# Kernel optimization log

Hardware: AMD Instinct MI355X
Metric: run time of the kernel (lower is better)

The kernel has to match this reference:

```python
import jax, jax.numpy as jnp
import numpy as np

DIM = 1024
N_HEADS = 16
HEAD_DIM = DIM // N_HEADS
LN_EPS = 1e-5


def layer_norm(x, gamma, beta, eps=LN_EPS):
    mu = jnp.mean(x, axis=-1, keepdims=True)
    var = jnp.var(x, axis=-1, keepdims=True)
    return (x - mu) * jax.lax.rsqrt(var + eps) * gamma + beta


def setup_inputs() -> dict:
    key = jax.random.key(0)
    ks = jax.random.split(key, 12)
    B, Nq, Nc, D = 2, 1024, 4096, DIM
    s = 1.0 / np.sqrt(D)  # torch Linear default init scale (uniform bound)
    inp = {
        "query": jax.random.normal(ks[0], (B, Nq, D), jnp.float32),
        "context": jax.random.normal(ks[1], (B, Nc, D), jnp.float32),
        "wq": jax.random.uniform(ks[2], (D, D), jnp.float32, -s, s),
        "bq": jax.random.uniform(ks[3], (D,), jnp.float32, -s, s),
        "wk": jax.random.uniform(ks[4], (D, D), jnp.float32, -s, s),
        "bk": jax.random.uniform(ks[5], (D,), jnp.float32, -s, s),
        "wv": jax.random.uniform(ks[6], (D, D), jnp.float32, -s, s),
        "bv": jax.random.uniform(ks[7], (D,), jnp.float32, -s, s),
        "wo": jax.random.uniform(ks[8], (D, D), jnp.float32, -s, s),
        "bo": jax.random.uniform(ks[9], (D,), jnp.float32, -s, s),
        "g_q": jnp.ones((D,), jnp.float32),
        "b_q": jnp.zeros((D,), jnp.float32),
        "g_kv": jnp.ones((D,), jnp.float32),
        "b_kv": jnp.zeros((D,), jnp.float32),
    }
    return inp


def reference(query, context, wq, bq, wk, bk, wv, bv, wo, bo, g_q, b_q, g_kv, b_kv):
    B, Nq, D = query.shape
    Nc = context.shape[1]
    H, Hd = N_HEADS, HEAD_DIM

    qn = layer_norm(query, g_q, b_q)        # [B,Nq,D]
    cn = layer_norm(context, g_kv, b_kv)    # [B,Nc,D]

    # torch Linear: y = x @ W.T + b; weights here stored as [out,in]
    Q = (jnp.einsum('bnd,ed->bne', qn, wq) + bq).reshape(B, Nq, H, Hd)
    K = (jnp.einsum('bnd,ed->bne', cn, wk) + bk).reshape(B, Nc, H, Hd)
    V = (jnp.einsum('bnd,ed->bne', cn, wv) + bv).reshape(B, Nc, H, Hd)

    scale = 1.0 / np.sqrt(Hd)
    scores = jnp.einsum('bqhd,bkhd->bhqk', Q, K) * scale  # [B,H,Nq,Nc]
    attn = jax.nn.softmax(scores, axis=-1)
    out = jnp.einsum('bhqk,bkhd->bqhd', attn, V).reshape(B, Nq, D)

    return qn + (jnp.einsum('bnd,ed->bne', out, wo) + bo)
```

## Files before the change

### kernel.cpp

```cpp
#include <hip/hip_runtime.h>

typedef unsigned short u16;
typedef __attribute__((ext_vector_type(8))) __bf16 bf16x8;
typedef __attribute__((ext_vector_type(4))) float f32x4;

struct alignas(8) U16x4 { u16 x, y, z, w; };

#define MFMA16(a, b, c) __builtin_amdgcn_mfma_f32_16x16x32_bf16(a, b, c, 0, 0, 0)

__device__ __forceinline__ u16 f2bf(float f) {
    union { float f; unsigned u; } v; v.f = f;
    unsigned r = v.u + 0x7fffu + ((v.u >> 16) & 1u);
    return (u16)(r >> 16);
}

__device__ __forceinline__ unsigned cvt_pk_bf16(float lo, float hi) {
    unsigned r;
    asm("v_cvt_pk_bf16_f32 %0, %1, %2" : "=v"(r) : "v"(lo), "v"(hi));
    return r;
}

__device__ __forceinline__ float fexp2(float x) {
    float r;
    asm("v_exp_f32 %0, %1" : "=v"(r) : "v"(x));
    return r;
}

__device__ __forceinline__ void gload_lds16(const void* g, void* l) {
    __builtin_amdgcn_global_load_lds(
        (__attribute__((address_space(1))) void*)g,
        (__attribute__((address_space(3))) void*)l, 16, 0, 0);
}

__global__ __launch_bounds__(256)
void prep(const float* __restrict__ query, const float* __restrict__ context,
          const float* __restrict__ g_q, const float* __restrict__ b_q,
          const float* __restrict__ g_kv, const float* __restrict__ b_kv,
          float* __restrict__ qn32, u16* __restrict__ qnb, u16* __restrict__ cnb,
          const float4* __restrict__ w0, const float4* __restrict__ w1,
          const float4* __restrict__ w2, const float4* __restrict__ w3,
          U16x4* __restrict__ o0, U16x4* __restrict__ o1,
          U16x4* __restrict__ o2, U16x4* __restrict__ o3)
{
    const int blk = blockIdx.x;
    if (blk < 2560) {
        const float *x, *g, *be; float* y32; u16* y16; int rb;
        if (blk < 512) { x = query;   g = g_q;  be = b_q;  y32 = qn32;    y16 = qnb; rb = blk; }
        else           { x = context; g = g_kv; be = b_kv; y32 = nullptr; y16 = cnb; rb = blk - 512; }
        const int wid = threadIdx.x >> 6, lane = threadIdx.x & 63;
        const size_t row = (size_t)rb * 4 + wid;
        const float4* xr = (const float4*)(x + row * 1024);
        float4 v[4];
        float s = 0.f, ss = 0.f;
#pragma unroll
        for (int i = 0; i < 4; ++i) {
            v[i] = xr[i * 64 + lane];
            s  += (v[i].x + v[i].y) + (v[i].z + v[i].w);
            ss += (v[i].x * v[i].x + v[i].y * v[i].y) + (v[i].z * v[i].z + v[i].w * v[i].w);
        }
#pragma unroll
        for (int o = 32; o; o >>= 1) { s += __shfl_xor(s, o, 64); ss += __shfl_xor(ss, o, 64); }
        const float mu = s * (1.f / 1024.f);
        const float rstd = rsqrtf(ss * (1.f / 1024.f) - mu * mu + 1e-5f);
#pragma unroll
        for (int i = 0; i < 4; ++i) {
            float4 gv = ((const float4*)g)[i * 64 + lane];
            float4 bv = ((const float4*)be)[i * 64 + lane];
            float4 o;
            o.x = (v[i].x - mu) * rstd * gv.x + bv.x;
            o.y = (v[i].y - mu) * rstd * gv.y + bv.y;
            o.z = (v[i].z - mu) * rstd * gv.z + bv.z;
            o.w = (v[i].w - mu) * rstd * gv.w + bv.w;
            if (y32) ((float4*)(y32 + row * 1024))[i * 64 + lane] = o;
            U16x4 pk = { f2bf(o.x), f2bf(o.y), f2bf(o.z), f2bf(o.w) };
            ((U16x4*)(y16 + row * 1024))[i * 64 + lane] = pk;
        }
    } else {
        const int i = (blk - 2560) * 256 + threadIdx.x;
        float4 v;
        v = w0[i]; o0[i] = { f2bf(v.x), f2bf(v.y), f2bf(v.z), f2bf(v.w) };
        v = w1[i]; o1[i] = { f2bf(v.x), f2bf(v.y), f2bf(v.z), f2bf(v.w) };
        v = w2[i]; o2[i] = { f2bf(v.x), f2bf(v.y), f2bf(v.z), f2bf(v.w) };
        v = w3[i]; o3[i] = { f2bf(v.x), f2bf(v.y), f2bf(v.z), f2bf(v.w) };
    }
}

__global__ __launch_bounds__(512, 4)
void gemm_kv(const u16* __restrict__ A, const u16* __restrict__ Wk,
             const u16* __restrict__ Wv, const float* __restrict__ bkp,
             const float* __restrict__ bvp, u16* __restrict__ Kout,
             u16* __restrict__ Vt)
{
    constexpr int K = 1024, N = 1024, BK = 64;
    __shared__ __align__(16) u16 sA[128 * BK];
    __shared__ __align__(16) u16 sK[128 * BK];
    __shared__ __align__(16) u16 sV[128 * BK];
    const int tid = threadIdx.x, wid = tid >> 6, lane = tid & 63;
    const int lr = lane & 15, lg = lane >> 4;
    const int wr = wid >> 2, wc = wid & 3;
    const int row0 = blockIdx.x * 128, col0 = blockIdx.y * 128;
    const int srow = wid * 8 + (lane >> 3), scol = (lane & 7) * 8;

    const u16* Ag = A  + (size_t)(row0 + srow) * K + scol;
    const u16* Kg = Wk + (size_t)(col0 + srow) * K + scol;
    const u16* Vg = Wv + (size_t)(col0 + srow) * K + scol;

    f32x4 ka[4][2], va[4][2];
#pragma unroll
    for (int m = 0; m < 4; ++m)
#pragma unroll
        for (int n = 0; n < 2; ++n) {
            ka[m][n] = (f32x4){0.f, 0.f, 0.f, 0.f};
            va[m][n] = (f32x4){0.f, 0.f, 0.f, 0.f};
        }

    for (int k0 = 0; k0 < K; k0 += BK) {
        __syncthreads();
#pragma unroll
        for (int i = 0; i < 2; ++i) {
            gload_lds16(Ag + (size_t)i * 64 * K + k0, (char*)sA + i * 8192 + wid * 1024);
            gload_lds16(Kg + (size_t)i * 64 * K + k0, (char*)sK + i * 8192 + wid * 1024);
            gload_lds16(Vg + (size_t)i * 64 * K + k0, (char*)sV + i * 8192 + wid * 1024);
        }
        __syncthreads();
#pragma unroll
        for (int kk = 0; kk < 2; ++kk) {
            bf16x8 af[4], bk[2], bv[2];
#pragma unroll
            for (int m = 0; m < 4; ++m)
                af[m] = *(const bf16x8*)&sA[(wr * 64 + m * 16 + lr) * BK + kk * 32 + lg * 8];
#pragma unroll
            for (int n = 0; n < 2; ++n) {
                bk[n] = *(const bf16x8*)&sK[(wc * 32 + n * 16 + lr) * BK + kk * 32 + lg * 8];
                bv[n] = *(const bf16x8*)&sV[(wc * 32 + n * 16 + lr) * BK + kk * 32 + lg * 8];
            }
#pragma unroll
            for (int m = 0; m < 4; ++m)
#pragma unroll
                for (int n = 0; n < 2; ++n) {
                    ka[m][n] = MFMA16(af[m], bk[n], ka[m][n]);
                    va[m][n] = MFMA16(af[m], bv[n], va[m][n]);
                }
        }
    }

#pragma unroll
    for (int m = 0; m < 4; ++m) {
#pragma unroll
        for (int n = 0; n < 2; ++n) {
            const int r = row0 + wr * 64 + m * 16 + lg * 4;
            const int c = col0 + wc * 32 + n * 16 + lr;
            const float kb = bkp[c], vb = bvp[c];
#pragma unroll
            for (int j = 0; j < 4; ++j)
                Kout[(size_t)(r + j) * N + c] = f2bf(ka[m][n][j] + kb);
            const size_t base = ((size_t)(r >> 12) * 1024 + c) * 4096 + (r & 4095);
            U16x4 pk = { f2bf(va[m][n][0] + vb), f2bf(va[m][n][1] + vb),
                         f2bf(va[m][n][2] + vb), f2bf(va[m][n][3] + vb) };
            *(U16x4*)&Vt[base] = pk;
        }
    }
}

template<int MODE>
__global__ __launch_bounds__(256)
void gemm_bt64(const u16* __restrict__ A, const u16* __restrict__ W,
               const float* __restrict__ bias, const float* __restrict__ resid,
               void* __restrict__ Cp, int M, int N, int K, float alpha)
{
    constexpr int BK = 64;
    __shared__ __align__(16) u16 sA[64 * BK];
    __shared__ __align__(16) u16 sB[128 * BK];
    const int tid = threadIdx.x, wid = tid >> 6, lane = tid & 63;
    const int lr = lane & 15, lg = lane >> 4;
    const int wr = wid >> 1, wc = wid & 1;
    const int row0 = blockIdx.x * 64, col0 = blockIdx.y * 128;
    const int srow = wid * 8 + (lane >> 3), scol = (lane & 7) * 8;

    const u16* Ag = A + (size_t)(row0 + srow) * K + scol;
    const u16* Wg = W + (size_t)(col0 + srow) * K + scol;

    f32x4 acc[2][4];
#pragma unroll
    for (int m = 0; m < 2; ++m)
#pragma unroll
        for (int n = 0; n < 4; ++n) acc[m][n] = (f32x4){0.f, 0.f, 0.f, 0.f};

    for (int k0 = 0; k0 < K; k0 += BK) {
        __syncthreads();
#pragma unroll
        for (int i = 0; i < 2; ++i)
            gload_lds16(Ag + (size_t)i * 32 * K + k0, (char*)sA + i * 4096 + wid * 1024);
#pragma unroll
        for (int i = 0; i < 4; ++i)
            gload_lds16(Wg + (size_t)i * 32 * K + k0, (char*)sB + i * 4096 + wid * 1024);
        __syncthreads();
#pragma unroll
        for (int kk = 0; kk < 2; ++kk) {
            bf16x8 af[2], bfr[4];
#pragma unroll
            for (int m = 0; m < 2; ++m)
                af[m] = *(const bf16x8*)&sA[(wr * 32 + m * 16 + lr) * BK + kk * 32 + lg * 8];
#pragma unroll
            for (int n = 0; n < 4; ++n)
                bfr[n] = *(const bf16x8*)&sB[(wc * 64 + n * 16 + lr) * BK + kk * 32 + lg * 8];
#pragma unroll
            for (int m = 0; m < 2; ++m)
#pragma unroll
                for (int n = 0; n < 4; ++n)
                    acc[m][n] = MFMA16(af[m], bfr[n], acc[m][n]);
        }
    }

#pragma unroll
    for (int m = 0; m < 2; ++m) {
#pragma unroll
        for (int n = 0; n < 4; ++n) {
            const int r = row0 + wr * 32 + m * 16 + lg * 4;
            const int c = col0 + wc * 64 + n * 16 + lr;
            const float bv = bias[c];
            if constexpr (MODE == 0) {
                u16* C = (u16*)Cp;
#pragma unroll
                for (int j = 0; j < 4; ++j)
                    C[(size_t)(r + j) * N + c] = f2bf((acc[m][n][j] + bv) * alpha);
            } else {
                float* C = (float*)Cp;
#pragma unroll
                for (int j = 0; j < 4; ++j)
                    C[(size_t)(r + j) * N + c] =
                        (acc[m][n][j] + bv) * alpha + resid[(size_t)(r + j) * N + c];
            }
        }
    }
}

__global__ __launch_bounds__(512, 4)
void attn_fwd(const u16* __restrict__ Q, const u16* __restrict__ Kg,
              const u16* __restrict__ Vt, u16* __restrict__ O)
{
    constexpr int D = 1024, CSTR = 19;
    __shared__ __align__(16) char smem[81920];

    const int tid = threadIdx.x, wid = tid >> 6, lane = tid & 63;
    const int grp = wid >> 2, w = wid & 3;
    const int lr = lane & 15, lg = lane >> 4;
    const int rs = lr & 7;
    const int pkey = (lr & 7) << 4;

    const int fid = blockIdx.x;
    const int wkid = (fid & 7) * 64 + (fid >> 3);
    const int qblk = wkid & 15, h = (wkid >> 4) & 15, b = wkid >> 8;
    const int q0 = qblk * 64 + w * 16;

    const u16* Qrow = Q + (size_t)(b * 1024 + q0 + lr) * D + h * 64;
    const bf16x8 qf0 = *(const bf16x8*)(Qrow + lg * 8);
    const bf16x8 qf1 = *(const bf16x8*)(Qrow + 32 + lg * 8);

    const int srow = w * 8 + (lane >> 3);
    const int scol = ((lane & 7) ^ (srow & 7)) * 8;
    const u16* kp = Kg + (size_t)(b * 4096 + grp * 2048 + srow) * D + h * 64 + scol;
    const u16* vp = Vt + ((size_t)(b * 16 + h) * 64 + srow) * 4096 + grp * 2048 + scol;

    char* sProw = smem + 65536 + wid * 2048 + lr * 128;

    f32x4 po[4];
#pragma unroll
    for (int df = 0; df < 4; ++df) po[df] = (f32x4){0.f, 0.f, 0.f, 0.f};
    float m = -INFINITY, l = 0.f;
    bf16x8 vr0, vr1, vr2, vr3, vr4, vr5, vr6, vr7;

    auto pv_step = [&]() {
        bf16x8 pf0 = *(const bf16x8*)(sProw + ((lg * 16) ^ pkey));
        bf16x8 pf1 = *(const bf16x8*)(sProw + ((64 + lg * 16) ^ pkey));
        po[0] = MFMA16(vr0, pf0, po[0]);
        po[1] = MFMA16(vr1, pf0, po[1]);
        po[2] = MFMA16(vr2, pf0, po[2]);
        po[3] = MFMA16(vr3, pf0, po[3]);
        po[0] = MFMA16(vr4, pf1, po[0]);
        po[1] = MFMA16(vr5, pf1, po[1]);
        po[2] = MFMA16(vr6, pf1, po[2]);
        po[3] = MFMA16(vr7, pf1, po[3]);
    };

    {
        char* kd = smem + grp * 8192 + w * 1024;
        char* vd = smem + 32768 + grp * 8192 + w * 1024;
        gload_lds16(kp,                      kd);
        gload_lds16(kp + (size_t)32 * D,     kd + 4096);
        gload_lds16(vp,                      vd);
        gload_lds16(vp + (size_t)32 * 4096,  vd + 4096);
        kp += (size_t)64 * D; vp += 64;
    }
    asm volatile("s_waitcnt vmcnt(0)" ::: "memory");
    asm volatile("s_barrier" ::: "memory");

    for (int t = 0; t < 32; ++t) {
        const int cur = t & 1;
        if (t < 31) {
            char* kd = smem + (cur ^ 1) * 16384 + grp * 8192 + w * 1024;
            char* vd = smem + 32768 + (cur ^ 1) * 16384 + grp * 8192 + w * 1024;
            gload_lds16(kp,                      kd);
            gload_lds16(kp + (size_t)32 * D,     kd + 4096);
            gload_lds16(vp,                      vd);
            gload_lds16(vp + (size_t)32 * 4096,  vd + 4096);
            kp += (size_t)64 * D; vp += 64;
        }

        const u16* kb = (const u16*)(smem + cur * 16384 + grp * 8192);
        const u16* vb = (const u16*)(smem + 32768 + cur * 16384 + grp * 8192);

        __builtin_amdgcn_s_setprio(1);
        if (t > 0) pv_step();

        f32x4 s4[4];
#pragma unroll
        for (int f = 0; f < 4; ++f) {
            const int r = f * 16 + lr;
            bf16x8 k0v = *(const bf16x8*)&kb[r * 64 + (lg ^ rs) * 8];
            bf16x8 k1v = *(const bf16x8*)&kb[r * 64 + ((lg + 4) ^ rs) * 8];
            f32x4 z = (f32x4){0.f, 0.f, 0.f, 0.f};
            z = MFMA16(k0v, qf0, z);
            s4[f] = MFMA16(k1v, qf1, z);
        }
        __builtin_amdgcn_s_setprio(0);

        vr0 = *(const bf16x8*)&vb[(0 * 16 + lr) * 64 + ((0 + lg) ^ rs) * 8];
        vr1 = *(const bf16x8*)&vb[(1 * 16 + lr) * 64 + ((0 + lg) ^ rs) * 8];
        vr2 = *(const bf16x8*)&vb[(2 * 16 + lr) * 64 + ((0 + lg) ^ rs) * 8];
        vr3 = *(const bf16x8*)&vb[(3 * 16 + lr) * 64 + ((0 + lg) ^ rs) * 8];
        vr4 = *(const bf16x8*)&vb[(0 * 16 + lr) * 64 + ((4 + lg) ^ rs) * 8];
        vr5 = *(const bf16x8*)&vb[(1 * 16 + lr) * 64 + ((4 + lg) ^ rs) * 8];
        vr6 = *(const bf16x8*)&vb[(2 * 16 + lr) * 64 + ((4 + lg) ^ rs) * 8];
        vr7 = *(const bf16x8*)&vb[(3 * 16 + lr) * 64 + ((4 + lg) ^ rs) * 8];

        float pmax = fmaxf(fmaxf(fmaxf(s4[0][0], s4[0][1]), fmaxf(s4[0][2], s4[0][3])),
                     fmaxf(fmaxf(fmaxf(s4[1][0], s4[1][1]), fmaxf(s4[1][2], s4[1][3])),
                     fmaxf(fmaxf(fmaxf(s4[2][0], s4[2][1]), fmaxf(s4[2][2], s4[2][3])),
                           fmaxf(fmaxf(s4[3][0], s4[3][1]), fmaxf(s4[3][2], s4[3][3])))));
        if (!__all(pmax <= m)) {
            float tmax = fmaxf(pmax, __shfl_xor(pmax, 16, 64));
            tmax = fmaxf(tmax, __shfl_xor(tmax, 32, 64));
            const float mn = fmaxf(m, tmax);
            const float corr = fexp2(m - mn);
            l *= corr;
#pragma unroll
            for (int df = 0; df < 4; ++df) po[df] *= corr;
            m = mn;
        }
        float lsum = 0.f;
        uint2 pk[4];
#pragma unroll
        for (int f = 0; f < 4; ++f) {
            float p0 = fexp2(s4[f][0] - m);
            float p1 = fexp2(s4[f][1] - m);
            float p2 = fexp2(s4[f][2] - m);
            float p3 = fexp2(s4[f][3] - m);
            lsum += (p0 + p1) + (p2 + p3);
            pk[f].x = cvt_pk_bf16(p0, p1);
            pk[f].y = cvt_pk_bf16(p2, p3);
        }
        l += lsum;

#pragma unroll
        for (int f = 0; f < 4; ++f)
            *(uint2*)(sProw + ((f * 32 + lg * 8) ^ pkey)) = pk[f];

        asm volatile("s_waitcnt vmcnt(0) lgkmcnt(0)" ::: "memory");
        asm volatile("s_barrier" ::: "memory");
    }

    pv_step();

    l += __shfl_xor(l, 16, 64);
    l += __shfl_xor(l, 32, 64);

    float* cb = (float*)smem;
    if (grp == 1) {
        float* dst = cb + (size_t)(w * 64 + lane) * CSTR;
        dst[0] = m; dst[1] = l;
#pragma unroll
        for (int df = 0; df < 4; ++df)
#pragma unroll
            for (int j = 0; j < 4; ++j) dst[2 + df * 4 + j] = po[df][j];
    }
    __syncthreads();
    if (grp == 0) {
        const float* src = cb + (size_t)(w * 64 + lane) * CSTR;
        const float m1 = src[0], l1 = src[1];
        const float M = fmaxf(m, m1);
        const float c0 = fexp2(m - M), c1 = fexp2(m1 - M);
        const float rl = 1.f / (l * c0 + l1 * c1);
        u16* Orow = O + (size_t)(b * 1024 + q0 + lr) * D + h * 64;
#pragma unroll
        for (int df = 0; df < 4; ++df) {
            U16x4 opk = { f2bf((po[df][0] * c0 + src[2 + df * 4 + 0] * c1) * rl),
                          f2bf((po[df][1] * c0 + src[2 + df * 4 + 1] * c1) * rl),
                          f2bf((po[df][2] * c0 + src[2 + df * 4 + 2] * c1) * rl),
                          f2bf((po[df][3] * c0 + src[2 + df * 4 + 3] * c1) * rl) };
            *(U16x4*)&Orow[df * 16 + lg * 4] = opk;
        }
    }
}

extern "C" void kernel_launch(void* const* d_in, const int* in_sizes, int n_in,
                              void* d_out, int out_size, void* d_ws, size_t ws_size,
                              hipStream_t stream)
{
    const float* query   = (const float*)d_in[0];
    const float* context = (const float*)d_in[1];
    const float* wq = (const float*)d_in[2];
    const float* bq = (const float*)d_in[3];
    const float* wk = (const float*)d_in[4];
    const float* bk = (const float*)d_in[5];
    const float* wv = (const float*)d_in[6];
    const float* bv = (const float*)d_in[7];
    const float* wo = (const float*)d_in[8];
    const float* bo = (const float*)d_in[9];
    const float* g_q  = (const float*)d_in[10];
    const float* b_q  = (const float*)d_in[11];
    const float* g_kv = (const float*)d_in[12];
    const float* b_kv = (const float*)d_in[13];

    char* p = (char*)d_ws;
    auto alloc = [&](size_t bytes) { char* r = p; p += (bytes + 255) & ~(size_t)255; return r; };
    u16*   wqb  = (u16*)alloc(1024 * 1024 * 2);
    u16*   wkb  = (u16*)alloc(1024 * 1024 * 2);
    u16*   wvb  = (u16*)alloc(1024 * 1024 * 2);
    u16*   wob  = (u16*)alloc(1024 * 1024 * 2);
    float* qn32 = (float*)alloc((size_t)2048 * 1024 * 4);
    u16*   qnb  = (u16*)alloc((size_t)2048 * 1024 * 2);
    u16*   cnb  = (u16*)alloc((size_t)8192 * 1024 * 2);
    u16*   Qb   = (u16*)alloc((size_t)2048 * 1024 * 2);
    u16*   Kb   = (u16*)alloc((size_t)8192 * 1024 * 2);
    u16*   Vtb  = (u16*)alloc((size_t)8192 * 1024 * 2);
    u16*   AOb  = (u16*)alloc((size_t)2048 * 1024 * 2);

    prep<<<3584, 256, 0, stream>>>(query, context, g_q, b_q, g_kv, b_kv,
                                   qn32, qnb, cnb,
                                   (const float4*)wq, (const float4*)wk,
                                   (const float4*)wv, (const float4*)wo,
                                   (U16x4*)wqb, (U16x4*)wkb, (U16x4*)wvb, (U16x4*)wob);

    gemm_bt64<0><<<dim3(32, 8), 256, 0, stream>>>(qnb, wqb, bq, nullptr, Qb, 2048, 1024, 1024, 0.18033688f);
    gemm_kv<<<dim3(64, 8), 512, 0, stream>>>(cnb, wkb, wvb, bk, bv, Kb, Vtb);

    attn_fwd<<<dim3(512), 512, 0, stream>>>(Qb, Kb, Vtb, AOb);

    gemm_bt64<1><<<dim3(32, 8), 256, 0, stream>>>(AOb, wob, bo, qn32, d_out, 2048, 1024, 1024, 1.0f);
}
```

Baseline: 164.6 us.

## Process two query tiles per wave in attention, halving block threads

Each wave in the attention kernel now handles 32 query rows (two 16-row tiles) instead of 16, with 4 waves per block instead of 8. Every K and V fragment read from shared memory is reused for two MFMAs, which cuts LDS traffic per FLOP. The software-pipelined PV step from the previous iteration is replaced by an in-iteration PV computation, so the s_setprio interleaving is dropped. In exchange, register pressure roughly doubles for the accumulators and there are fewer waves per CU to hide latency.

```diff
diff --git a/kernel.cpp b/kernel.cpp
--- a/kernel.cpp
+++ b/kernel.cpp
@@ -235,15 +235,15 @@
     }
 }
 
-__global__ __launch_bounds__(512, 4)
+__global__ __launch_bounds__(256, 2)
 void attn_fwd(const u16* __restrict__ Q, const u16* __restrict__ Kg,
               const u16* __restrict__ Vt, u16* __restrict__ O)
 {
-    constexpr int D = 1024, CSTR = 19;
+    constexpr int D = 1024, CSTR = 36;
     __shared__ __align__(16) char smem[81920];
 
     const int tid = threadIdx.x, wid = tid >> 6, lane = tid & 63;
-    const int grp = wid >> 2, w = wid & 3;
+    const int grp = wid >> 1, w = wid & 1;
     const int lr = lane & 15, lg = lane >> 4;
     const int rs = lr & 7;
     const int pkey = (lr & 7) << 4;
@@ -251,154 +251,161 @@
     const int fid = blockIdx.x;
     const int wkid = (fid & 7) * 64 + (fid >> 3);
     const int qblk = wkid & 15, h = (wkid >> 4) & 15, b = wkid >> 8;
-    const int q0 = qblk * 64 + w * 16;
-
-    const u16* Qrow = Q + (size_t)(b * 1024 + q0 + lr) * D + h * 64;
-    const bf16x8 qf0 = *(const bf16x8*)(Qrow + lg * 8);
-    const bf16x8 qf1 = *(const bf16x8*)(Qrow + 32 + lg * 8);
-
-    const int srow = w * 8 + (lane >> 3);
-    const int scol = ((lane & 7) ^ (srow & 7)) * 8;
-    const u16* kp = Kg + (size_t)(b * 4096 + grp * 2048 + srow) * D + h * 64 + scol;
-    const u16* vp = Vt + ((size_t)(b * 16 + h) * 64 + srow) * 4096 + grp * 2048 + scol;
-
-    char* sProw = smem + 65536 + wid * 2048 + lr * 128;
-
-    f32x4 po[4];
-#pragma unroll
-    for (int df = 0; df < 4; ++df) po[df] = (f32x4){0.f, 0.f, 0.f, 0.f};
-    float m = -INFINITY, l = 0.f;
-    bf16x8 vr0, vr1, vr2, vr3, vr4, vr5, vr6, vr7;
-
-    auto pv_step = [&]() {
-        bf16x8 pf0 = *(const bf16x8*)(sProw + ((lg * 16) ^ pkey));
-        bf16x8 pf1 = *(const bf16x8*)(sProw + ((64 + lg * 16) ^ pkey));
-        po[0] = MFMA16(vr0, pf0, po[0]);
-        po[1] = MFMA16(vr1, pf0, po[1]);
-        po[2] = MFMA16(vr2, pf0, po[2]);
-        po[3] = MFMA16(vr3, pf0, po[3]);
-        po[0] = MFMA16(vr4, pf1, po[0]);
-        po[1] = MFMA16(vr5, pf1, po[1]);
-        po[2] = MFMA16(vr6, pf1, po[2]);
-        po[3] = MFMA16(vr7, pf1, po[3]);
+    const int q0 = qblk * 64 + w * 32;
+
+    const u16* Qbase = Q + (size_t)(b * 1024 + q0 + lr) * D + h * 64;
+    bf16x8 qf[2][2];
+    qf[0][0] = *(const bf16x8*)(Qbase + lg * 8);
+    qf[0][1] = *(const bf16x8*)(Qbase + 32 + lg * 8);
+    qf[1][0] = *(const bf16x8*)(Qbase + (size_t)16 * D + lg * 8);
+    qf[1][1] = *(const bf16x8*)(Qbase + (size_t)16 * D + 32 + lg * 8);
+
+    const int srow0 = lane >> 3;
+    const int scol = ((lane & 7) ^ srow0) * 8;
+    const u16* kp = Kg + (size_t)(b * 4096 + grp * 2048 + w * 32 + srow0) * D + h * 64 + scol;
+    const u16* vp = Vt + ((size_t)(b * 16 + h) * 64 + w * 32 + srow0) * 4096 + grp * 2048 + scol;
+
+    char* sPw = smem + 65536 + wid * 4096;
+
+    f32x4 po[4][2];
+#pragma unroll
+    for (int df = 0; df < 4; ++df) {
+        po[df][0] = (f32x4){0.f, 0.f, 0.f, 0.f};
+        po[df][1] = (f32x4){0.f, 0.f, 0.f, 0.f};
+    }
+    float m0 = -INFINITY, m1 = -INFINITY, l0 = 0.f, l1 = 0.f;
+
+    auto stage = [&](int buf, int kv0) {
+        char* kd = smem + buf * 16384 + grp * 8192 + w * 4096;
+        char* vd = smem + 32768 + buf * 16384 + grp * 8192 + w * 4096;
+#pragma unroll
+        for (int i = 0; i < 4; ++i) {
+            gload_lds16(kp + (size_t)(kv0 + i * 8) * D,     kd + i * 1024);
+            gload_lds16(vp + (size_t)(i * 8) * 4096 + kv0,  vd + i * 1024);
+        }
     };
 
-    {
-        char* kd = smem + grp * 8192 + w * 1024;
-        char* vd = smem + 32768 + grp * 8192 + w * 1024;
-        gload_lds16(kp,                      kd);
-        gload_lds16(kp + (size_t)32 * D,     kd + 4096);
-        gload_lds16(vp,                      vd);
-        gload_lds16(vp + (size_t)32 * 4096,  vd + 4096);
-        kp += (size_t)64 * D; vp += 64;
-    }
+    stage(0, 0);
     asm volatile("s_waitcnt vmcnt(0)" ::: "memory");
     asm volatile("s_barrier" ::: "memory");
 
     for (int t = 0; t < 32; ++t) {
         const int cur = t & 1;
-        if (t < 31) {
-            char* kd = smem + (cur ^ 1) * 16384 + grp * 8192 + w * 1024;
-            char* vd = smem + 32768 + (cur ^ 1) * 16384 + grp * 8192 + w * 1024;
-            gload_lds16(kp,                      kd);
-            gload_lds16(kp + (size_t)32 * D,     kd + 4096);
-            gload_lds16(vp,                      vd);
-            gload_lds16(vp + (size_t)32 * 4096,  vd + 4096);
-            kp += (size_t)64 * D; vp += 64;
-        }
+        if (t < 31) stage(cur ^ 1, (t + 1) * 64);
 
         const u16* kb = (const u16*)(smem + cur * 16384 + grp * 8192);
         const u16* vb = (const u16*)(smem + 32768 + cur * 16384 + grp * 8192);
 
-        __builtin_amdgcn_s_setprio(1);
-        if (t > 0) pv_step();
-
-        f32x4 s4[4];
+        f32x4 s4[4][2];
 #pragma unroll
         for (int f = 0; f < 4; ++f) {
             const int r = f * 16 + lr;
             bf16x8 k0v = *(const bf16x8*)&kb[r * 64 + (lg ^ rs) * 8];
             bf16x8 k1v = *(const bf16x8*)&kb[r * 64 + ((lg + 4) ^ rs) * 8];
-            f32x4 z = (f32x4){0.f, 0.f, 0.f, 0.f};
-            z = MFMA16(k0v, qf0, z);
-            s4[f] = MFMA16(k1v, qf1, z);
-        }
-        __builtin_amdgcn_s_setprio(0);
-
-        vr0 = *(const bf16x8*)&vb[(0 * 16 + lr) * 64 + ((0 + lg) ^ rs) * 8];
-        vr1 = *(const bf16x8*)&vb[(1 * 16 + lr) * 64 + ((0 + lg) ^ rs) * 8];
-        vr2 = *(const bf16x8*)&vb[(2 * 16 + lr) * 64 + ((0 + lg) ^ rs) * 8];
-        vr3 = *(const bf16x8*)&vb[(3 * 16 + lr) * 64 + ((0 + lg) ^ rs) * 8];
-        vr4 = *(const bf16x8*)&vb[(0 * 16 + lr) * 64 + ((4 + lg) ^ rs) * 8];
-        vr5 = *(const bf16x8*)&vb[(1 * 16 + lr) * 64 + ((4 + lg) ^ rs) * 8];
-        vr6 = *(const bf16x8*)&vb[(2 * 16 + lr) * 64 + ((4 + lg) ^ rs) * 8];
-        vr7 = *(const bf16x8*)&vb[(3 * 16 + lr) * 64 + ((4 + lg) ^ rs) * 8];
-
-        float pmax = fmaxf(fmaxf(fmaxf(s4[0][0], s4[0][1]), fmaxf(s4[0][2], s4[0][3])),
-                     fmaxf(fmaxf(fmaxf(s4[1][0], s4[1][1]), fmaxf(s4[1][2], s4[1][3])),
-                     fmaxf(fmaxf(fmaxf(s4[2][0], s4[2][1]), fmaxf(s4[2][2], s4[2][3])),
-                           fmaxf(fmaxf(s4[3][0], s4[3][1]), fmaxf(s4[3][2], s4[3][3])))));
-        if (!__all(pmax <= m)) {
-            float tmax = fmaxf(pmax, __shfl_xor(pmax, 16, 64));
-            tmax = fmaxf(tmax, __shfl_xor(tmax, 32, 64));
-            const float mn = fmaxf(m, tmax);
-            const float corr = fexp2(m - mn);
-            l *= corr;
-#pragma unroll
-            for (int df = 0; df < 4; ++df) po[df] *= corr;
-            m = mn;
-        }
-        float lsum = 0.f;
-        uint2 pk[4];
+#pragma unroll
+            for (int qc = 0; qc < 2; ++qc) {
+                f32x4 z = (f32x4){0.f, 0.f, 0.f, 0.f};
+                z = MFMA16(k0v, qf[qc][0], z);
+                s4[f][qc] = MFMA16(k1v, qf[qc][1], z);
+            }
+        }
+
+        float pm0 = s4[0][0][0], pm1 = s4[0][1][0];
 #pragma unroll
         for (int f = 0; f < 4; ++f) {
-            float p0 = fexp2(s4[f][0] - m);
-            float p1 = fexp2(s4[f][1] - m);
-            float p2 = fexp2(s4[f][2] - m);
-            float p3 = fexp2(s4[f][3] - m);
-            lsum += (p0 + p1) + (p2 + p3);
-            pk[f].x = cvt_pk_bf16(p0, p1);
-            pk[f].y = cvt_pk_bf16(p2, p3);
-        }
-        l += lsum;
-
-#pragma unroll
-        for (int f = 0; f < 4; ++f)
-            *(uint2*)(sProw + ((f * 32 + lg * 8) ^ pkey)) = pk[f];
-
-        asm volatile("s_waitcnt vmcnt(0) lgkmcnt(0)" ::: "memory");
+            pm0 = fmaxf(pm0, fmaxf(fmaxf(s4[f][0][0], s4[f][0][1]), fmaxf(s4[f][0][2], s4[f][0][3])));
+            pm1 = fmaxf(pm1, fmaxf(fmaxf(s4[f][1][0], s4[f][1][1]), fmaxf(s4[f][1][2], s4[f][1][3])));
+        }
+        if (!__all(pm0 <= m0 && pm1 <= m1)) {
+            float t0 = fmaxf(pm0, __shfl_xor(pm0, 16, 64));
+            t0 = fmaxf(t0, __shfl_xor(t0, 32, 64));
+            float t1 = fmaxf(pm1, __shfl_xor(pm1, 16, 64));
+            t1 = fmaxf(t1, __shfl_xor(t1, 32, 64));
+            const float mn0 = fmaxf(m0, t0), mn1 = fmaxf(m1, t1);
+            const float c0 = fexp2(m0 - mn0), c1 = fexp2(m1 - mn1);
+            l0 *= c0; l1 *= c1;
+#pragma unroll
+            for (int df = 0; df < 4; ++df) { po[df][0] *= c0; po[df][1] *= c1; }
+            m0 = mn0; m1 = mn1;
+        }
+        float ls0 = 0.f, ls1 = 0.f;
+        uint2 pk[4][2];
+#pragma unroll
+        for (int f = 0; f < 4; ++f) {
+            float a0 = fexp2(s4[f][0][0] - m0), a1 = fexp2(s4[f][0][1] - m0);
+            float a2 = fexp2(s4[f][0][2] - m0), a3 = fexp2(s4[f][0][3] - m0);
+            ls0 += (a0 + a1) + (a2 + a3);
+            pk[f][0].x = cvt_pk_bf16(a0, a1);
+            pk[f][0].y = cvt_pk_bf16(a2, a3);
+            float b0 = fexp2(s4[f][1][0] - m1), b1 = fexp2(s4[f][1][1] - m1);
+            float b2 = fexp2(s4[f][1][2] - m1), b3 = fexp2(s4[f][1][3] - m1);
+            ls1 += (b0 + b1) + (b2 + b3);
+            pk[f][1].x = cvt_pk_bf16(b0, b1);
+            pk[f][1].y = cvt_pk_bf16(b2, b3);
+        }
+        l0 += ls0; l1 += ls1;
+
+#pragma unroll
+        for (int f = 0; f < 4; ++f) {
+            *(uint2*)(sPw + lr * 128        + ((f * 32 + lg * 8) ^ pkey)) = pk[f][0];
+            *(uint2*)(sPw + (16 + lr) * 128 + ((f * 32 + lg * 8) ^ pkey)) = pk[f][1];
+        }
+
+#pragma unroll
+        for (int c = 0; c < 2; ++c) {
+            bf16x8 pf0 = *(const bf16x8*)(sPw + lr * 128        + ((c * 64 + lg * 16) ^ pkey));
+            bf16x8 pf1 = *(const bf16x8*)(sPw + (16 + lr) * 128 + ((c * 64 + lg * 16) ^ pkey));
+#pragma unroll
+            for (int df = 0; df < 4; ++df) {
+                const int r = df * 16 + lr;
+                bf16x8 vf = *(const bf16x8*)&vb[r * 64 + ((c * 4 + lg) ^ rs) * 8];
+                po[df][0] = MFMA16(vf, pf0, po[df][0]);
+                po[df][1] = MFMA16(vf, pf1, po[df][1]);
+            }
+        }
+
+        asm volatile("s_waitcnt vmcnt(0)" ::: "memory");
         asm volatile("s_barrier" ::: "memory");
     }
 
-    pv_step();
-
-    l += __shfl_xor(l, 16, 64);
-    l += __shfl_xor(l, 32, 64);
+    l0 += __shfl_xor(l0, 16, 64); l0 += __shfl_xor(l0, 32, 64);
+    l1 += __shfl_xor(l1, 16, 64); l1 += __shfl_xor(l1, 32, 64);
 
     float* cb = (float*)smem;
     if (grp == 1) {
         float* dst = cb + (size_t)(w * 64 + lane) * CSTR;
-        dst[0] = m; dst[1] = l;
+        dst[0] = m0; dst[1] = m1; dst[2] = l0; dst[3] = l1;
 #pragma unroll
         for (int df = 0; df < 4; ++df)
 #pragma unroll
-            for (int j = 0; j < 4; ++j) dst[2 + df * 4 + j] = po[df][j];
+            for (int qc = 0; qc < 2; ++qc)
+#pragma unroll
+                for (int j = 0; j < 4; ++j)
+                    dst[4 + (df * 2 + qc) * 4 + j] = po[df][qc][j];
     }
     __syncthreads();
     if (grp == 0) {
         const float* src = cb + (size_t)(w * 64 + lane) * CSTR;
-        const float m1 = src[0], l1 = src[1];
-        const float M = fmaxf(m, m1);
-        const float c0 = fexp2(m - M), c1 = fexp2(m1 - M);
-        const float rl = 1.f / (l * c0 + l1 * c1);
+        const float sm0 = src[0], sm1 = src[1], sl0 = src[2], sl1 = src[3];
+        const float M0 = fmaxf(m0, sm0), M1 = fmaxf(m1, sm1);
+        const float a0 = fexp2(m0 - M0), b0 = fexp2(sm0 - M0);
+        const float a1 = fexp2(m1 - M1), b1 = fexp2(sm1 - M1);
+        const float rl0 = 1.f / (l0 * a0 + sl0 * b0);
+        const float rl1 = 1.f / (l1 * a1 + sl1 * b1);
         u16* Orow = O + (size_t)(b * 1024 + q0 + lr) * D + h * 64;
 #pragma unroll
-        for (int df = 0; df < 4; ++df) {
-            U16x4 opk = { f2bf((po[df][0] * c0 + src[2 + df * 4 + 0] * c1) * rl),
-                          f2bf((po[df][1] * c0 + src[2 + df * 4 + 1] * c1) * rl),
-                          f2bf((po[df][2] * c0 + src[2 + df * 4 + 2] * c1) * rl),
-                          f2bf((po[df][3] * c0 + src[2 + df * 4 + 3] * c1) * rl) };
-            *(U16x4*)&Orow[df * 16 + lg * 4] = opk;
+        for (int qc = 0; qc < 2; ++qc) {
+            const float ca = qc ? a1 : a0, cbb = qc ? b1 : b0, rl = qc ? rl1 : rl0;
+            u16* orow = Orow + (size_t)qc * 16 * D;
+#pragma unroll
+            for (int df = 0; df < 4; ++df) {
+                const float* sv = src + 4 + (df * 2 + qc) * 4;
+                U16x4 opk = { f2bf((po[df][qc][0] * ca + sv[0] * cbb) * rl),
+                              f2bf((po[df][qc][1] * ca + sv[1] * cbb) * rl),
+                              f2bf((po[df][qc][2] * ca + sv[2] * cbb) * rl),
+                              f2bf((po[df][qc][3] * ca + sv[3] * cbb) * rl) };
+                *(U16x4*)&orow[df * 16 + lg * 4] = opk;
+            }
         }
     }
 }
@@ -445,7 +452,7 @@
     gemm_bt64<0><<<dim3(32, 8), 256, 0, stream>>>(qnb, wqb, bq, nullptr, Qb, 2048, 1024, 1024, 0.18033688f);
     gemm_kv<<<dim3(64, 8), 512, 0, stream>>>(cnb, wkb, wvb, bk, bv, Kb, Vtb);
 
-    attn_fwd<<<dim3(512), 512, 0, stream>>>(Qb, Kb, Vtb, AOb);
+    attn_fwd<<<dim3(512), 256, 0, stream>>>(Qb, Kb, Vtb, AOb);
 
     gemm_bt64<1><<<dim3(32, 8), 256, 0, stream>>>(AOb, wob, bo, qn32, d_out, 2048, 1024, 1024, 1.0f);
 }
```

After: 164.8 us. No clear change (+0.1%).

## Halve attention KV tile to 32 keys, cutting LDS and registers for higher occupancy

Applied to the files above, without the earlier changes.

The attention kernel now processes 32 keys per step instead of 64. This halves the LDS footprint from 80KB to 40KB and drops the eight persistent V-fragment registers, so launch bounds can request 8 blocks per CU instead of 4. The PV product is now done inside the same step, right after P is written, using a per-wave private P buffer with a new swizzle. The software-pipelined PV overlap and the setprio hints are removed. The cost is twice as many barriers and softmax rescale checks per row, and less MFMA work per sync.

```diff
diff --git a/kernel.cpp b/kernel.cpp
--- a/kernel.cpp
+++ b/kernel.cpp
@@ -235,18 +235,18 @@
     }
 }
 
-__global__ __launch_bounds__(512, 4)
+__global__ __launch_bounds__(512, 8)
 void attn_fwd(const u16* __restrict__ Q, const u16* __restrict__ Kg,
               const u16* __restrict__ Vt, u16* __restrict__ O)
 {
     constexpr int D = 1024, CSTR = 19;
-    __shared__ __align__(16) char smem[81920];
+    __shared__ __align__(16) char smem[40960];
 
     const int tid = threadIdx.x, wid = tid >> 6, lane = tid & 63;
     const int grp = wid >> 2, w = wid & 3;
     const int lr = lane & 15, lg = lane >> 4;
     const int rs = lr & 7;
-    const int pkey = (lr & 7) << 4;
+    const int vk = (lr >> 1) & 3;
 
     const int fid = blockIdx.x;
     const int wkid = (fid & 7) * 64 + (fid >> 3);
@@ -260,62 +260,31 @@
     const int srow = w * 8 + (lane >> 3);
     const int scol = ((lane & 7) ^ (srow & 7)) * 8;
     const u16* kp = Kg + (size_t)(b * 4096 + grp * 2048 + srow) * D + h * 64 + scol;
-    const u16* vp = Vt + ((size_t)(b * 16 + h) * 64 + srow) * 4096 + grp * 2048 + scol;
-
-    char* sProw = smem + 65536 + wid * 2048 + lr * 128;
+    const int vrow = w * 16 + (lane >> 2);
+    const int vcol = ((lane & 3) ^ ((vrow >> 1) & 3)) * 8;
+    const u16* vp = Vt + ((size_t)(b * 16 + h) * 64 + vrow) * 4096 + grp * 2048 + vcol;
+
+    char* sPw = smem + 32768 + wid * 1024;
 
     f32x4 po[4];
 #pragma unroll
     for (int df = 0; df < 4; ++df) po[df] = (f32x4){0.f, 0.f, 0.f, 0.f};
     float m = -INFINITY, l = 0.f;
-    bf16x8 vr0, vr1, vr2, vr3, vr4, vr5, vr6, vr7;
-
-    auto pv_step = [&]() {
-        bf16x8 pf0 = *(const bf16x8*)(sProw + ((lg * 16) ^ pkey));
-        bf16x8 pf1 = *(const bf16x8*)(sProw + ((64 + lg * 16) ^ pkey));
-        po[0] = MFMA16(vr0, pf0, po[0]);
-        po[1] = MFMA16(vr1, pf0, po[1]);
-        po[2] = MFMA16(vr2, pf0, po[2]);
-        po[3] = MFMA16(vr3, pf0, po[3]);
-        po[0] = MFMA16(vr4, pf1, po[0]);
-        po[1] = MFMA16(vr5, pf1, po[1]);
-        po[2] = MFMA16(vr6, pf1, po[2]);
-        po[3] = MFMA16(vr7, pf1, po[3]);
+
+    auto stage = [&](int buf, int kv0) {
+        gload_lds16(kp + (size_t)kv0 * D, smem + buf * 8192 + grp * 4096 + w * 1024);
+        gload_lds16(vp + kv0, smem + 16384 + buf * 8192 + grp * 4096 + w * 1024);
     };
 
-    {
-        char* kd = smem + grp * 8192 + w * 1024;
-        char* vd = smem + 32768 + grp * 8192 + w * 1024;
-        gload_lds16(kp,                      kd);
-        gload_lds16(kp + (size_t)32 * D,     kd + 4096);
-        gload_lds16(vp,                      vd);
-        gload_lds16(vp + (size_t)32 * 4096,  vd + 4096);
-        kp += (size_t)64 * D; vp += 64;
-    }
-    asm volatile("s_waitcnt vmcnt(0)" ::: "memory");
-    asm volatile("s_barrier" ::: "memory");
-
-    for (int t = 0; t < 32; ++t) {
-        const int cur = t & 1;
-        if (t < 31) {
-            char* kd = smem + (cur ^ 1) * 16384 + grp * 8192 + w * 1024;
-            char* vd = smem + 32768 + (cur ^ 1) * 16384 + grp * 8192 + w * 1024;
-            gload_lds16(kp,                      kd);
-            gload_lds16(kp + (size_t)32 * D,     kd + 4096);
-            gload_lds16(vp,                      vd);
-            gload_lds16(vp + (size_t)32 * 4096,  vd + 4096);
-            kp += (size_t)64 * D; vp += 64;
-        }
-
-        const u16* kb = (const u16*)(smem + cur * 16384 + grp * 8192);
-        const u16* vb = (const u16*)(smem + 32768 + cur * 16384 + grp * 8192);
-
-        __builtin_amdgcn_s_setprio(1);
-        if (t > 0) pv_step();
-
-        f32x4 s4[4];
-#pragma unroll
-        for (int f = 0; f < 4; ++f) {
+    auto step = [&](int t, int cur) {
+        if (t < 63) stage(cur ^ 1, (t + 1) * 32);
+
+        const u16* kb = (const u16*)(smem + cur * 8192 + grp * 4096);
+        const u16* vb = (const u16*)(smem + 16384 + cur * 8192 + grp * 4096);
+
+        f32x4 s4[2];
+#pragma unroll
+        for (int f = 0; f < 2; ++f) {
             const int r = f * 16 + lr;
             bf16x8 k0v = *(const bf16x8*)&kb[r * 64 + (lg ^ rs) * 8];
             bf16x8 k1v = *(const bf16x8*)&kb[r * 64 + ((lg + 4) ^ rs) * 8];
@@ -323,21 +292,9 @@
             z = MFMA16(k0v, qf0, z);
             s4[f] = MFMA16(k1v, qf1, z);
         }
-        __builtin_amdgcn_s_setprio(0);
-
-        vr0 = *(const bf16x8*)&vb[(0 * 16 + lr) * 64 + ((0 + lg) ^ rs) * 8];
-        vr1 = *(const bf16x8*)&vb[(1 * 16 + lr) * 64 + ((0 + lg) ^ rs) * 8];
-        vr2 = *(const bf16x8*)&vb[(2 * 16 + lr) * 64 + ((0 + lg) ^ rs) * 8];
-        vr3 = *(const bf16x8*)&vb[(3 * 16 + lr) * 64 + ((0 + lg) ^ rs) * 8];
-        vr4 = *(const bf16x8*)&vb[(0 * 16 + lr) * 64 + ((4 + lg) ^ rs) * 8];
-        vr5 = *(const bf16x8*)&vb[(1 * 16 + lr) * 64 + ((4 + lg) ^ rs) * 8];
-        vr6 = *(const bf16x8*)&vb[(2 * 16 + lr) * 64 + ((4 + lg) ^ rs) * 8];
-        vr7 = *(const bf16x8*)&vb[(3 * 16 + lr) * 64 + ((4 + lg) ^ rs) * 8];
 
         float pmax = fmaxf(fmaxf(fmaxf(s4[0][0], s4[0][1]), fmaxf(s4[0][2], s4[0][3])),
-                     fmaxf(fmaxf(fmaxf(s4[1][0], s4[1][1]), fmaxf(s4[1][2], s4[1][3])),
-                     fmaxf(fmaxf(fmaxf(s4[2][0], s4[2][1]), fmaxf(s4[2][2], s4[2][3])),
-                           fmaxf(fmaxf(s4[3][0], s4[3][1]), fmaxf(s4[3][2], s4[3][3])))));
+                           fmaxf(fmaxf(s4[1][0], s4[1][1]), fmaxf(s4[1][2], s4[1][3])));
         if (!__all(pmax <= m)) {
             float tmax = fmaxf(pmax, __shfl_xor(pmax, 16, 64));
             tmax = fmaxf(tmax, __shfl_xor(tmax, 32, 64));
@@ -349,9 +306,9 @@
             m = mn;
         }
         float lsum = 0.f;
-        uint2 pk[4];
-#pragma unroll
-        for (int f = 0; f < 4; ++f) {
+        uint2 pk[2];
+#pragma unroll
+        for (int f = 0; f < 2; ++f) {
             float p0 = fexp2(s4[f][0] - m);
             float p1 = fexp2(s4[f][1] - m);
             float p2 = fexp2(s4[f][2] - m);
@@ -363,14 +320,29 @@
         l += lsum;
 
 #pragma unroll
-        for (int f = 0; f < 4; ++f)
-            *(uint2*)(sProw + ((f * 32 + lg * 8) ^ pkey)) = pk[f];
-
-        asm volatile("s_waitcnt vmcnt(0) lgkmcnt(0)" ::: "memory");
+        for (int f = 0; f < 2; ++f)
+            *(uint2*)(sPw + lr * 64 + ((2 * f + (lg >> 1)) ^ vk) * 16 + (lg & 1) * 8) = pk[f];
+
+        bf16x8 pf = *(const bf16x8*)(sPw + lr * 64 + (lg ^ vk) * 16);
+#pragma unroll
+        for (int df = 0; df < 4; ++df) {
+            const int r = df * 16 + lr;
+            bf16x8 vf = *(const bf16x8*)&vb[r * 32 + (lg ^ vk) * 8];
+            po[df] = MFMA16(vf, pf, po[df]);
+        }
+
+        asm volatile("s_waitcnt vmcnt(0)" ::: "memory");
         asm volatile("s_barrier" ::: "memory");
-    }
-
-    pv_step();
+    };
+
+    stage(0, 0);
+    asm volatile("s_waitcnt vmcnt(0)" ::: "memory");
+    asm volatile("s_barrier" ::: "memory");
+
+    for (int tt = 0; tt < 32; ++tt) {
+        step(tt * 2, 0);
+        step(tt * 2 + 1, 1);
+    }
 
     l += __shfl_xor(l, 16, 64);
     l += __shfl_xor(l, 32, 64);
```

New measurement: 168.5 us. 2.3% more time.

## Swizzle GEMM LDS tiles and un-pipeline attention PV step

Applied to the files above, without the earlier changes.

Applies an XOR swizzle to the column index of the shared-memory tiles in both GEMM kernels, for stores and fragment reads alike, so that MFMA fragment loads avoid LDS bank conflicts. In the attention kernel, the software-pipelined PV step (V fragments held in registers and applied one iteration late at raised priority) is replaced by an in-iteration PV computation that reads V and P from LDS right after P is written. The attention change cuts register pressure and the setprio tricks but gives up the overlap of PV MFMAs with the next QK step. It also relaxes the end-of-iteration wait to vmcnt only.

```diff
diff --git a/kernel.cpp b/kernel.cpp
--- a/kernel.cpp
+++ b/kernel.cpp
@@ -97,9 +97,11 @@
     __shared__ __align__(16) u16 sV[128 * BK];
     const int tid = threadIdx.x, wid = tid >> 6, lane = tid & 63;
     const int lr = lane & 15, lg = lane >> 4;
+    const int rk = lr & 7;
     const int wr = wid >> 2, wc = wid & 3;
     const int row0 = blockIdx.x * 128, col0 = blockIdx.y * 128;
-    const int srow = wid * 8 + (lane >> 3), scol = (lane & 7) * 8;
+    const int srow = wid * 8 + (lane >> 3);
+    const int scol = ((lane & 7) ^ (srow & 7)) * 8;
 
     const u16* Ag = A  + (size_t)(row0 + srow) * K + scol;
     const u16* Kg = Wk + (size_t)(col0 + srow) * K + scol;
@@ -128,11 +130,11 @@
             bf16x8 af[4], bk[2], bv[2];
 #pragma unroll
             for (int m = 0; m < 4; ++m)
-                af[m] = *(const bf16x8*)&sA[(wr * 64 + m * 16 + lr) * BK + kk * 32 + lg * 8];
+                af[m] = *(const bf16x8*)&sA[(wr * 64 + m * 16 + lr) * BK + ((kk * 4 + lg) ^ rk) * 8];
 #pragma unroll
             for (int n = 0; n < 2; ++n) {
-                bk[n] = *(const bf16x8*)&sK[(wc * 32 + n * 16 + lr) * BK + kk * 32 + lg * 8];
-                bv[n] = *(const bf16x8*)&sV[(wc * 32 + n * 16 + lr) * BK + kk * 32 + lg * 8];
+                bk[n] = *(const bf16x8*)&sK[(wc * 32 + n * 16 + lr) * BK + ((kk * 4 + lg) ^ rk) * 8];
+                bv[n] = *(const bf16x8*)&sV[(wc * 32 + n * 16 + lr) * BK + ((kk * 4 + lg) ^ rk) * 8];
             }
 #pragma unroll
             for (int m = 0; m < 4; ++m)
@@ -173,9 +175,11 @@
     __shared__ __align__(16) u16 sB[128 * BK];
     const int tid = threadIdx.x, wid = tid >> 6, lane = tid & 63;
     const int lr = lane & 15, lg = lane >> 4;
+    const int rk = lr & 7;
     const int wr = wid >> 1, wc = wid & 1;
     const int row0 = blockIdx.x * 64, col0 = blockIdx.y * 128;
-    const int srow = wid * 8 + (lane >> 3), scol = (lane & 7) * 8;
+    const int srow = wid * 8 + (lane >> 3);
+    const int scol = ((lane & 7) ^ (srow & 7)) * 8;
 
     const u16* Ag = A + (size_t)(row0 + srow) * K + scol;
     const u16* Wg = W + (size_t)(col0 + srow) * K + scol;
@@ -200,10 +204,10 @@
             bf16x8 af[2], bfr[4];
 #pragma unroll
             for (int m = 0; m < 2; ++m)
-                af[m] = *(const bf16x8*)&sA[(wr * 32 + m * 16 + lr) * BK + kk * 32 + lg * 8];
+                af[m] = *(const bf16x8*)&sA[(wr * 32 + m * 16 + lr) * BK + ((kk * 4 + lg) ^ rk) * 8];
 #pragma unroll
             for (int n = 0; n < 4; ++n)
-                bfr[n] = *(const bf16x8*)&sB[(wc * 64 + n * 16 + lr) * BK + kk * 32 + lg * 8];
+                bfr[n] = *(const bf16x8*)&sB[(wc * 64 + n * 16 + lr) * BK + ((kk * 4 + lg) ^ rk) * 8];
 #pragma unroll
             for (int m = 0; m < 2; ++m)
 #pragma unroll
@@ -249,8 +253,8 @@
     const int pkey = (lr & 7) << 4;
 
     const int fid = blockIdx.x;
-    const int wkid = (fid & 7) * 64 + (fid >> 3);
-    const int qblk = wkid & 15, h = (wkid >> 4) & 15, b = wkid >> 8;
+    const int wk = (fid & 7) * 64 + (fid >> 3);
+    const int qblk = wk & 15, h = (wk >> 4) & 15, b = wk >> 8;
     const int q0 = qblk * 64 + w * 16;
 
     const u16* Qrow = Q + (size_t)(b * 1024 + q0 + lr) * D + h * 64;
@@ -268,20 +272,6 @@
 #pragma unroll
     for (int df = 0; df < 4; ++df) po[df] = (f32x4){0.f, 0.f, 0.f, 0.f};
     float m = -INFINITY, l = 0.f;
-    bf16x8 vr0, vr1, vr2, vr3, vr4, vr5, vr6, vr7;
-
-    auto pv_step = [&]() {
-        bf16x8 pf0 = *(const bf16x8*)(sProw + ((lg * 16) ^ pkey));
-        bf16x8 pf1 = *(const bf16x8*)(sProw + ((64 + lg * 16) ^ pkey));
-        po[0] = MFMA16(vr0, pf0, po[0]);
-        po[1] = MFMA16(vr1, pf0, po[1]);
-        po[2] = MFMA16(vr2, pf0, po[2]);
-        po[3] = MFMA16(vr3, pf0, po[3]);
-        po[0] = MFMA16(vr4, pf1, po[0]);
-        po[1] = MFMA16(vr5, pf1, po[1]);
-        po[2] = MFMA16(vr6, pf1, po[2]);
-        po[3] = MFMA16(vr7, pf1, po[3]);
-    };
 
     {
         char* kd = smem + grp * 8192 + w * 1024;
@@ -310,9 +300,6 @@
         const u16* kb = (const u16*)(smem + cur * 16384 + grp * 8192);
         const u16* vb = (const u16*)(smem + 32768 + cur * 16384 + grp * 8192);
 
-        __builtin_amdgcn_s_setprio(1);
-        if (t > 0) pv_step();
-
         f32x4 s4[4];
 #pragma unroll
         for (int f = 0; f < 4; ++f) {
@@ -323,16 +310,6 @@
             z = MFMA16(k0v, qf0, z);
             s4[f] = MFMA16(k1v, qf1, z);
         }
-        __builtin_amdgcn_s_setprio(0);
-
-        vr0 = *(const bf16x8*)&vb[(0 * 16 + lr) * 64 + ((0 + lg) ^ rs) * 8];
-        vr1 = *(const bf16x8*)&vb[(1 * 16 + lr) * 64 + ((0 + lg) ^ rs) * 8];
-        vr2 = *(const bf16x8*)&vb[(2 * 16 + lr) * 64 + ((0 + lg) ^ rs) * 8];
-        vr3 = *(const bf16x8*)&vb[(3 * 16 + lr) * 64 + ((0 + lg) ^ rs) * 8];
-        vr4 = *(const bf16x8*)&vb[(0 * 16 + lr) * 64 + ((4 + lg) ^ rs) * 8];
-        vr5 = *(const bf16x8*)&vb[(1 * 16 + lr) * 64 + ((4 + lg) ^ rs) * 8];
-        vr6 = *(const bf16x8*)&vb[(2 * 16 + lr) * 64 + ((4 + lg) ^ rs) * 8];
-        vr7 = *(const bf16x8*)&vb[(3 * 16 + lr) * 64 + ((4 + lg) ^ rs) * 8];
 
         float pmax = fmaxf(fmaxf(fmaxf(s4[0][0], s4[0][1]), fmaxf(s4[0][2], s4[0][3])),
                      fmaxf(fmaxf(fmaxf(s4[1][0], s4[1][1]), fmaxf(s4[1][2], s4[1][3])),
@@ -366,11 +343,20 @@
         for (int f = 0; f < 4; ++f)
             *(uint2*)(sProw + ((f * 32 + lg * 8) ^ pkey)) = pk[f];
 
-        asm volatile("s_waitcnt vmcnt(0) lgkmcnt(0)" ::: "memory");
+#pragma unroll
+        for (int c = 0; c < 2; ++c) {
+            bf16x8 pf = *(const bf16x8*)(sProw + ((c * 64 + lg * 16) ^ pkey));
+#pragma unroll
+            for (int df = 0; df < 4; ++df) {
+                const int r = df * 16 + lr;
+                bf16x8 vf = *(const bf16x8*)&vb[r * 64 + ((c * 4 + lg) ^ rs) * 8];
+                po[df] = MFMA16(vf, pf, po[df]);
+            }
+        }
+
+        asm volatile("s_waitcnt vmcnt(0)" ::: "memory");
         asm volatile("s_barrier" ::: "memory");
     }
-
-    pv_step();
 
     l += __shfl_xor(l, 16, 64);
     l += __shfl_xor(l, 32, 64);
```

Measured after the change: 168.2 us. 1.02x slower.
